# Performance work log

Measured on AMD Instinct MI355X. Metric: run time of the kernel, lower is better.

Reference implementation:

```python
import jax, jax.numpy as jnp
import numpy as np

N_HEAD = 12
HEAD_SIZE = 64  # 768 / 12
SCALE = 1.0 / np.sqrt(HEAD_SIZE)


def setup_inputs() -> dict:
    key = jax.random.key(0)
    k1, k2, k3 = jax.random.split(key, 3)
    B, T, C = 8, 1024, 768
    x = jax.random.normal(k1, (B, T, C), dtype=jnp.float32)
    W_attn = jax.random.normal(k2, (C, 3 * C), dtype=jnp.float32) * 0.02
    b_attn = jax.random.normal(k3, (3 * C,), dtype=jnp.float32) * 0.02
    return {"x": x, "W_attn": W_attn, "b_attn": b_attn}


def reference(x, W_attn, b_attn):
    B, T, C = x.shape
    hs = C // N_HEAD
    qkv = x @ W_attn + b_attn                      # [B, T, 3C]
    q, k, v = jnp.split(qkv, 3, axis=-1)
    # [B, nh, T, hs]
    q = q.reshape(B, T, N_HEAD, hs).transpose(0, 2, 1, 3)
    k = k.reshape(B, T, N_HEAD, hs).transpose(0, 2, 1, 3)
    v = v.reshape(B, T, N_HEAD, hs).transpose(0, 2, 1, 3)
    scores = jnp.einsum('bhqd,bhkd->bhqk', q, k) * SCALE
    causal = jnp.tril(jnp.ones((T, T), dtype=bool))  # [T, T]
    # masked positions get -inf then relu -> 0; equivalent to where(mask, relu, 0)
    att = jnp.where(causal, jax.nn.relu(scores), 0.0)
    y = jnp.einsum('bhqk,bhkd->bhqd', att, v)      # [B, nh, T, hs]
    return y.transpose(0, 2, 1, 3).reshape(B, T, C)
```

## Files before the change

### kernel.cpp

```cpp
#include <hip/hip_runtime.h>
#include <stdint.h>

typedef __bf16 bf16;
typedef __attribute__((ext_vector_type(8))) __bf16 bf16x8;
typedef __attribute__((ext_vector_type(4))) __bf16 bf16x4;
typedef __attribute__((ext_vector_type(4))) float  f32x4;

#define ATT_SCALE 0.125f

__device__ __forceinline__ void async16(void* lds, const void* g) {
  __builtin_amdgcn_global_load_lds(
      (__attribute__((address_space(1))) void*)(void*)g,
      (__attribute__((address_space(3))) void*)lds,
      16, 0, 0);
}

__global__ void convert_x_kernel(const float* __restrict__ x, bf16* __restrict__ y) {
  size_t i = ((size_t)blockIdx.x * 256 + threadIdx.x) * 8;
  float4 a = *(const float4*)(x + i);
  float4 b = *(const float4*)(x + i + 4);
  bf16x8 o;
  o[0] = (bf16)a.x; o[1] = (bf16)a.y; o[2] = (bf16)a.z; o[3] = (bf16)a.w;
  o[4] = (bf16)b.x; o[5] = (bf16)b.y; o[6] = (bf16)b.z; o[7] = (bf16)b.w;
  *(bf16x8*)(y + i) = o;
}

__global__ void transpose_w_kernel(const float* __restrict__ W, bf16* __restrict__ Wt) {
  __shared__ float tile[32][33];
  int tx = threadIdx.x, ty = threadIdx.y;
  int n0 = blockIdx.x * 32, k0 = blockIdx.y * 32;
#pragma unroll
  for (int r = 0; r < 4; ++r)
    tile[ty + r * 8][tx] = W[(size_t)(k0 + ty + r * 8) * 2304 + n0 + tx];
  __syncthreads();
#pragma unroll
  for (int r = 0; r < 4; ++r)
    Wt[(size_t)(n0 + ty + r * 8) * 768 + k0 + tx] = (bf16)tile[tx][ty + r * 8];
}

__global__ void qkv_gemm_kernel(const bf16* __restrict__ A, const bf16* __restrict__ Bw,
                                const float* __restrict__ bias,
                                bf16* __restrict__ Qo, bf16* __restrict__ Ko,
                                bf16* __restrict__ Vo) {
  __shared__ __align__(16) char lds[32768];
  char* Al = lds;
  char* Bl = lds + 16384;

  const int tid  = threadIdx.x;
  const int wave = tid >> 6, lane = tid & 63;
  const int quad = lane >> 4, mn = lane & 15;
  const int wr = wave >> 1, wc = wave & 1;
  const int m0 = blockIdx.y * 128;
  const int n0 = blockIdx.x * 128;

  f32x4 acc[4][4] = {};

  const int lrow = lane >> 3;
  const int cg   = (lane & 7) ^ lrow;

  for (int kt = 0; kt < 768; kt += 64) {
#pragma unroll
    for (int u = 0; u < 4; ++u) {
      const int t   = wave * 4 + u;
      const int row = t * 8 + lrow;
      async16(Al + t * 1024 + lane * 16,
              A  + (size_t)(m0 + row) * 768 + kt + cg * 8);
      async16(Bl + t * 1024 + lane * 16,
              Bw + (size_t)(n0 + row) * 768 + kt + cg * 8);
    }
    __syncthreads();

#pragma unroll
    for (int s = 0; s < 2; ++s) {
      bf16x8 af[4], bfr[4];
      const int csw = ((s * 4 + quad) ^ (mn & 7)) * 16;
#pragma unroll
      for (int i = 0; i < 4; ++i) {
        af[i]  = *(const bf16x8*)(Al + (wr * 64 + i * 16 + mn) * 128 + csw);
        bfr[i] = *(const bf16x8*)(Bl + (wc * 64 + i * 16 + mn) * 128 + csw);
      }
#pragma unroll
      for (int i = 0; i < 4; ++i)
#pragma unroll
        for (int j = 0; j < 4; ++j)
          acc[i][j] = __builtin_amdgcn_mfma_f32_16x16x32_bf16(af[i], bfr[j], acc[i][j], 0, 0, 0);
    }
    __syncthreads();
  }

  const int ng    = n0 + wc * 64;
  const int third = ng / 768;
  const int nmod  = ng % 768;
  const float sc  = (third == 0) ? ATT_SCALE : 1.0f;
#pragma unroll
  for (int ct = 0; ct < 4; ++ct) {
    int n = nmod + ct * 16 + mn;
    int h = n >> 6, d = n & 63;
    float bv = bias[third * 768 + n];
#pragma unroll
    for (int rt = 0; rt < 4; ++rt) {
      int m  = m0 + wr * 64 + rt * 16 + quad * 4;
      int b  = m >> 10, t0 = m & 1023;
      size_t bh = (size_t)b * 12 + h;
      if (third == 2) {
        bf16x4 pk;
#pragma unroll
        for (int r = 0; r < 4; ++r) pk[r] = (bf16)(acc[rt][ct][r] + bv);
        *(bf16x4*)(Vo + (bh * 64 + d) * 1024 + t0) = pk;
      } else {
        bf16* dst = (third == 0 ? Qo : Ko) + (bh * 1024 + t0) * 64 + d;
#pragma unroll
        for (int r = 0; r < 4; ++r) dst[(size_t)r * 64] = (bf16)((acc[rt][ct][r] + bv) * sc);
      }
    }
  }
}

__global__ void attn_kernel(const bf16* __restrict__ Q, const bf16* __restrict__ K,
                            const bf16* __restrict__ Vt, float* __restrict__ out) {
  __shared__ __align__(16) char lds[55296];
  char* ldsS = lds + 36864;

  const int tid  = threadIdx.x;
  const int wave = tid >> 6, lane = tid & 63;
  const int quad = lane >> 4, mn = lane & 15;
  const int bh = blockIdx.x;
  const int qt = (int)gridDim.y - 1 - (int)blockIdx.y;
  const int q0 = qt * 128;
  const int jmax  = 2 * qt + 1;
  const int jdiag = 2 * qt + (wave >> 1);

  const bf16* Qbase = Q + ((size_t)bh * 1024 + q0 + wave * 32) * 64;
  bf16x8 qf[2][2];
#pragma unroll
  for (int i = 0; i < 2; ++i) {
    const bf16* Qrow = Qbase + (i * 16 + mn) * 64;
    qf[i][0] = *(const bf16x8*)(Qrow + quad * 8);
    qf[i][1] = *(const bf16x8*)(Qrow + 32 + quad * 8);
  }

  f32x4 yacc[2][4] = {};

  const int trow = tid >> 3;
  const int tcol = tid & 7;
  const bf16* Kg0 = K  + (size_t)bh * 65536;
  const bf16* Vg0 = Vt + (size_t)bh * 65536;

  bf16x8 r0 = *(const bf16x8*)(Kg0 + trow * 64 + tcol * 8);
  bf16x8 r1 = *(const bf16x8*)(Kg0 + (trow + 32) * 64 + tcol * 8);
  bf16x8 r2 = *(const bf16x8*)(Vg0 + (size_t)trow * 1024 + tcol * 8);
  bf16x8 r3 = *(const bf16x8*)(Vg0 + (size_t)(trow + 32) * 1024 + tcol * 8);

  for (int j = 0; j <= jmax; ++j) {
    char* bK = lds + (j & 1) * 18432;
    char* bV = bK + 9216;
    *(bf16x8*)(bK + trow * 144 + tcol * 16) = r0;
    *(bf16x8*)(bK + (trow + 32) * 144 + tcol * 16) = r1;
    *(bf16x8*)(bV + trow * 144 + tcol * 16) = r2;
    *(bf16x8*)(bV + (trow + 32) * 144 + tcol * 16) = r3;
    if (j < jmax) {
      const bf16* Kg = Kg0 + (size_t)(j + 1) * 4096;
      const bf16* Vg = Vg0 + (j + 1) * 64;
      r0 = *(const bf16x8*)(Kg + trow * 64 + tcol * 8);
      r1 = *(const bf16x8*)(Kg + (trow + 32) * 64 + tcol * 8);
      r2 = *(const bf16x8*)(Vg + (size_t)trow * 1024 + tcol * 8);
      r3 = *(const bf16x8*)(Vg + (size_t)(trow + 32) * 1024 + tcol * 8);
    }
    __syncthreads();

    if (j <= jdiag) {
      const bool diag = (j == jdiag);
#pragma unroll
      for (int ct = 0; ct < 4; ++ct) {
        bf16x8 kf0 = *(const bf16x8*)(bK + (ct * 16 + mn) * 144 + quad * 16);
        bf16x8 kf1 = *(const bf16x8*)(bK + (ct * 16 + mn) * 144 + 64 + quad * 16);
        int kkc = j * 64 + ct * 16 + mn;
#pragma unroll
        for (int i = 0; i < 2; ++i) {
          f32x4 a = {};
          a = __builtin_amdgcn_mfma_f32_16x16x32_bf16(qf[i][0], kf0, a, 0, 0, 0);
          a = __builtin_amdgcn_mfma_f32_16x16x32_bf16(qf[i][1], kf1, a, 0, 0, 0);
          int qr = q0 + wave * 32 + i * 16 + quad * 4;
#pragma unroll
          for (int r = 0; r < 4; ++r) {
            float v = a[r];
            v = v > 0.f ? v : 0.f;
            if (diag && kkc > qr + r) v = 0.f;
            ((bf16*)ldsS)[(wave * 32 + i * 16 + quad * 4 + r) * 72 + ct * 16 + mn] = (bf16)v;
          }
        }
      }
#pragma unroll
      for (int kb = 0; kb < 2; ++kb) {
        bf16x8 vf[4];
#pragma unroll
        for (int ct = 0; ct < 4; ++ct)
          vf[ct] = *(const bf16x8*)(bV + (ct * 16 + mn) * 144 + kb * 64 + quad * 16);
#pragma unroll
        for (int i = 0; i < 2; ++i) {
          bf16x8 sf = *(const bf16x8*)(ldsS + (wave * 32 + i * 16 + mn) * 144 + kb * 64 + quad * 16);
#pragma unroll
          for (int ct = 0; ct < 4; ++ct)
            yacc[i][ct] = __builtin_amdgcn_mfma_f32_16x16x32_bf16(sf, vf[ct], yacc[i][ct], 0, 0, 0);
        }
      }
    }
  }

  const int b = bh / 12, h = bh % 12;
#pragma unroll
  for (int i = 0; i < 2; ++i) {
    float* ob = out + ((size_t)b * 1024 + q0 + wave * 32 + i * 16 + quad * 4) * 768 + h * 64;
#pragma unroll
    for (int ct = 0; ct < 4; ++ct)
#pragma unroll
      for (int r = 0; r < 4; ++r)
        ob[(size_t)r * 768 + ct * 16 + mn] = yacc[i][ct][r];
  }
}

extern "C" void kernel_launch(void* const* d_in, const int* in_sizes, int n_in,
                              void* d_out, int out_size, void* d_ws, size_t ws_size,
                              hipStream_t stream) {
  const float* x    = (const float*)d_in[0];
  const float* W    = (const float*)d_in[1];
  const float* bias = (const float*)d_in[2];
  float* out = (float*)d_out;

  char* ws = (char*)d_ws;
  bf16* xb = (bf16*)(ws);
  bf16* Wt = (bf16*)(ws + 12582912);
  bf16* Qb = (bf16*)(ws + 16121856);
  bf16* Kb = (bf16*)(ws + 28704768);
  bf16* Vb = (bf16*)(ws + 41287680);

  convert_x_kernel<<<3072, 256, 0, stream>>>(x, xb);
  transpose_w_kernel<<<dim3(72, 24), dim3(32, 8), 0, stream>>>(W, Wt);
  qkv_gemm_kernel<<<dim3(18, 64), 256, 0, stream>>>(xb, Wt, bias, Qb, Kb, Vb);
  attn_kernel<<<dim3(96, 8), 256, 0, stream>>>(Qb, Kb, Vb, out);
}
```

Before: 151.4 us.

## Double-buffer QKV GEMM LDS and pair causal query tiles in attention

The QKV GEMM now stages the next K-slice into a second LDS buffer while computing on the current one, which removes one barrier per iteration and overlaps load with MFMA work. The attention kernel switches from 128-row query tiles to pairs of 64-row tiles (qt and 15-qt) per block, so every block does the same amount of causal work. It uses a single-buffered K/V LDS tile with more barriers and sets launch bounds to raise occupancy. The grid dimension in the launch is unchanged at 8, which matches 8 pairs of 16 tiles.

Measured after the change: 152.7 us. Within noise of the previous version (+0.8%).

```diff
diff --git a/kernel.cpp b/kernel.cpp
--- a/kernel.cpp
+++ b/kernel.cpp
@@ -42,9 +42,7 @@
                                 const float* __restrict__ bias,
                                 bf16* __restrict__ Qo, bf16* __restrict__ Ko,
                                 bf16* __restrict__ Vo) {
-  __shared__ __align__(16) char lds[32768];
-  char* Al = lds;
-  char* Bl = lds + 16384;
+  __shared__ __align__(16) char lds[65536];
 
   const int tid  = threadIdx.x;
   const int wave = tid >> 6, lane = tid & 63;
@@ -58,7 +56,9 @@
   const int lrow = lane >> 3;
   const int cg   = (lane & 7) ^ lrow;
 
-  for (int kt = 0; kt < 768; kt += 64) {
+  auto stage = [&](int kt, char* buf) {
+    char* Al = buf;
+    char* Bl = buf + 16384;
 #pragma unroll
     for (int u = 0; u < 4; ++u) {
       const int t   = wave * 4 + u;
@@ -68,7 +68,15 @@
       async16(Bl + t * 1024 + lane * 16,
               Bw + (size_t)(n0 + row) * 768 + kt + cg * 8);
     }
+  };
+
+  stage(0, lds);
+  int p = 0;
+  for (int kt = 0; kt < 768; kt += 64) {
     __syncthreads();
+    if (kt + 64 < 768) stage(kt + 64, lds + (p ^ 1) * 32768);
+    char* Al = lds + p * 32768;
+    char* Bl = Al + 16384;
 
 #pragma unroll
     for (int s = 0; s < 2; ++s) {
@@ -85,7 +93,7 @@
         for (int j = 0; j < 4; ++j)
           acc[i][j] = __builtin_amdgcn_mfma_f32_16x16x32_bf16(af[i], bfr[j], acc[i][j], 0, 0, 0);
     }
-    __syncthreads();
+    p ^= 1;
   }
 
   const int ng    = n0 + wc * 64;
@@ -116,49 +124,54 @@
   }
 }
 
-__global__ void attn_kernel(const bf16* __restrict__ Q, const bf16* __restrict__ K,
-                            const bf16* __restrict__ Vt, float* __restrict__ out) {
-  __shared__ __align__(16) char lds[55296];
-  char* ldsS = lds + 36864;
+__global__ __launch_bounds__(256, 4)
+void attn_kernel(const bf16* __restrict__ Q, const bf16* __restrict__ K,
+                 const bf16* __restrict__ Vt, float* __restrict__ out) {
+  __shared__ __align__(16) char lds[36864];
+  char* ldsK = lds;
+  char* ldsV = lds + 9216;
+  char* ldsS = lds + 18432;
 
   const int tid  = threadIdx.x;
   const int wave = tid >> 6, lane = tid & 63;
   const int quad = lane >> 4, mn = lane & 15;
-  const int bh = blockIdx.x;
-  const int qt = (int)gridDim.y - 1 - (int)blockIdx.y;
-  const int q0 = qt * 128;
-  const int jmax  = 2 * qt + 1;
-  const int jdiag = 2 * qt + (wave >> 1);
-
-  const bf16* Qbase = Q + ((size_t)bh * 1024 + q0 + wave * 32) * 64;
-  bf16x8 qf[2][2];
-#pragma unroll
-  for (int i = 0; i < 2; ++i) {
-    const bf16* Qrow = Qbase + (i * 16 + mn) * 64;
-    qf[i][0] = *(const bf16x8*)(Qrow + quad * 8);
-    qf[i][1] = *(const bf16x8*)(Qrow + 32 + quad * 8);
-  }
-
-  f32x4 yacc[2][4] = {};
+  const int bh  = blockIdx.x;
+  const int qta = blockIdx.y;
+  const int qtb = 15 - qta;
+  const int qa0 = qta * 64, qb0 = qtb * 64;
+
+  const bf16* Qg  = Q  + (size_t)bh * 65536;
+  const bf16* Kg0 = K  + (size_t)bh * 65536;
+  const bf16* Vg0 = Vt + (size_t)bh * 65536;
+
+  bf16x8 qfA[2], qfB[2];
+  {
+    const bf16* ra = Qg + (size_t)(qa0 + wave * 16 + mn) * 64;
+    qfA[0] = *(const bf16x8*)(ra + quad * 8);
+    qfA[1] = *(const bf16x8*)(ra + 32 + quad * 8);
+    const bf16* rb = Qg + (size_t)(qb0 + wave * 16 + mn) * 64;
+    qfB[0] = *(const bf16x8*)(rb + quad * 8);
+    qfB[1] = *(const bf16x8*)(rb + 32 + quad * 8);
+  }
+
+  f32x4 yA[4] = {}, yB[4] = {};
 
   const int trow = tid >> 3;
   const int tcol = tid & 7;
-  const bf16* Kg0 = K  + (size_t)bh * 65536;
-  const bf16* Vg0 = Vt + (size_t)bh * 65536;
 
   bf16x8 r0 = *(const bf16x8*)(Kg0 + trow * 64 + tcol * 8);
   bf16x8 r1 = *(const bf16x8*)(Kg0 + (trow + 32) * 64 + tcol * 8);
   bf16x8 r2 = *(const bf16x8*)(Vg0 + (size_t)trow * 1024 + tcol * 8);
   bf16x8 r3 = *(const bf16x8*)(Vg0 + (size_t)(trow + 32) * 1024 + tcol * 8);
 
-  for (int j = 0; j <= jmax; ++j) {
-    char* bK = lds + (j & 1) * 18432;
-    char* bV = bK + 9216;
-    *(bf16x8*)(bK + trow * 144 + tcol * 16) = r0;
-    *(bf16x8*)(bK + (trow + 32) * 144 + tcol * 16) = r1;
-    *(bf16x8*)(bV + trow * 144 + tcol * 16) = r2;
-    *(bf16x8*)(bV + (trow + 32) * 144 + tcol * 16) = r3;
-    if (j < jmax) {
+  for (int j = 0; j <= qtb; ++j) {
+    if (j) __syncthreads();
+    *(bf16x8*)(ldsK + trow * 144 + tcol * 16) = r0;
+    *(bf16x8*)(ldsK + (trow + 32) * 144 + tcol * 16) = r1;
+    *(bf16x8*)(ldsV + trow * 144 + tcol * 16) = r2;
+    *(bf16x8*)(ldsV + (trow + 32) * 144 + tcol * 16) = r3;
+    __syncthreads();
+    if (j < qtb) {
       const bf16* Kg = Kg0 + (size_t)(j + 1) * 4096;
       const bf16* Vg = Vg0 + (j + 1) * 64;
       r0 = *(const bf16x8*)(Kg + trow * 64 + tcol * 8);
@@ -166,56 +179,55 @@
       r2 = *(const bf16x8*)(Vg + (size_t)trow * 1024 + tcol * 8);
       r3 = *(const bf16x8*)(Vg + (size_t)(trow + 32) * 1024 + tcol * 8);
     }
-    __syncthreads();
-
-    if (j <= jdiag) {
-      const bool diag = (j == jdiag);
+
+    auto do_half = [&](const bf16x8* qf, f32x4* y, int half, int qrow0, bool diag) {
 #pragma unroll
       for (int ct = 0; ct < 4; ++ct) {
-        bf16x8 kf0 = *(const bf16x8*)(bK + (ct * 16 + mn) * 144 + quad * 16);
-        bf16x8 kf1 = *(const bf16x8*)(bK + (ct * 16 + mn) * 144 + 64 + quad * 16);
+        bf16x8 kf0 = *(const bf16x8*)(ldsK + (ct * 16 + mn) * 144 + quad * 16);
+        bf16x8 kf1 = *(const bf16x8*)(ldsK + (ct * 16 + mn) * 144 + 64 + quad * 16);
+        f32x4 a = {};
+        a = __builtin_amdgcn_mfma_f32_16x16x32_bf16(qf[0], kf0, a, 0, 0, 0);
+        a = __builtin_amdgcn_mfma_f32_16x16x32_bf16(qf[1], kf1, a, 0, 0, 0);
         int kkc = j * 64 + ct * 16 + mn;
 #pragma unroll
-        for (int i = 0; i < 2; ++i) {
-          f32x4 a = {};
-          a = __builtin_amdgcn_mfma_f32_16x16x32_bf16(qf[i][0], kf0, a, 0, 0, 0);
-          a = __builtin_amdgcn_mfma_f32_16x16x32_bf16(qf[i][1], kf1, a, 0, 0, 0);
-          int qr = q0 + wave * 32 + i * 16 + quad * 4;
-#pragma unroll
-          for (int r = 0; r < 4; ++r) {
-            float v = a[r];
-            v = v > 0.f ? v : 0.f;
-            if (diag && kkc > qr + r) v = 0.f;
-            ((bf16*)ldsS)[(wave * 32 + i * 16 + quad * 4 + r) * 72 + ct * 16 + mn] = (bf16)v;
-          }
+        for (int r = 0; r < 4; ++r) {
+          float v = a[r];
+          v = v > 0.f ? v : 0.f;
+          if (diag && kkc > qrow0 + quad * 4 + r) v = 0.f;
+          ((bf16*)ldsS)[(half * 64 + wave * 16 + quad * 4 + r) * 72 + ct * 16 + mn] = (bf16)v;
         }
       }
 #pragma unroll
       for (int kb = 0; kb < 2; ++kb) {
-        bf16x8 vf[4];
-#pragma unroll
-        for (int ct = 0; ct < 4; ++ct)
-          vf[ct] = *(const bf16x8*)(bV + (ct * 16 + mn) * 144 + kb * 64 + quad * 16);
-#pragma unroll
-        for (int i = 0; i < 2; ++i) {
-          bf16x8 sf = *(const bf16x8*)(ldsS + (wave * 32 + i * 16 + mn) * 144 + kb * 64 + quad * 16);
-#pragma unroll
-          for (int ct = 0; ct < 4; ++ct)
-            yacc[i][ct] = __builtin_amdgcn_mfma_f32_16x16x32_bf16(sf, vf[ct], yacc[i][ct], 0, 0, 0);
+        bf16x8 sf = *(const bf16x8*)(ldsS + (half * 64 + wave * 16 + mn) * 144 + kb * 64 + quad * 16);
+#pragma unroll
+        for (int ct = 0; ct < 4; ++ct) {
+          bf16x8 vf = *(const bf16x8*)(ldsV + (ct * 16 + mn) * 144 + kb * 64 + quad * 16);
+          y[ct] = __builtin_amdgcn_mfma_f32_16x16x32_bf16(sf, vf, y[ct], 0, 0, 0);
         }
       }
-    }
+    };
+
+    if (j <= qta) do_half(qfA, yA, 0, qa0 + wave * 16, j == qta);
+    do_half(qfB, yB, 1, qb0 + wave * 16, j == qtb);
   }
 
   const int b = bh / 12, h = bh % 12;
-#pragma unroll
-  for (int i = 0; i < 2; ++i) {
-    float* ob = out + ((size_t)b * 1024 + q0 + wave * 32 + i * 16 + quad * 4) * 768 + h * 64;
+  {
+    float* ob = out + ((size_t)b * 1024 + qa0 + wave * 16 + quad * 4) * 768 + h * 64;
 #pragma unroll
     for (int ct = 0; ct < 4; ++ct)
 #pragma unroll
       for (int r = 0; r < 4; ++r)
-        ob[(size_t)r * 768 + ct * 16 + mn] = yacc[i][ct][r];
+        ob[(size_t)r * 768 + ct * 16 + mn] = yA[ct][r];
+  }
+  {
+    float* ob = out + ((size_t)b * 1024 + qb0 + wave * 16 + quad * 4) * 768 + h * 64;
+#pragma unroll
+    for (int ct = 0; ct < 4; ++ct)
+#pragma unroll
+      for (int r = 0; r < 4; ++r)
+        ob[(size_t)r * 768 + ct * 16 + mn] = yB[ct][r];
   }
 }
 
```
